# Performance work log

Hardware: AMD Instinct MI355X
Metric: run time of the kernel (lower is better)

Reference implementation:

```python
import jax, jax.numpy as jnp
import numpy as np

B, K, V, D, H, S, KS = 4, 4, 32, 64, 4, 1024, 5
GROUPS = K * V  # 128


def setup_inputs() -> dict:
    key = jax.random.key(0)
    k1, k2 = jax.random.split(key, 2)
    x = jax.random.normal(k1, (B, GROUPS * 3, S), dtype=jnp.float32)
    # grouped causal conv weight: (out_ch, in_ch_per_group, ks) = (K*V*D*3, 3, KS)
    W = jax.random.normal(k2, (GROUPS * D * 3, 3, KS), dtype=jnp.float32) * 0.05
    b = jnp.zeros((GROUPS * D * 3,), dtype=jnp.float32)
    return {"x": x, "W": W, "b": b}


def reference(x, W, b):
    temperature = 1.0
    dk = D // H
    # --- TCN (stand-in): causal grouped conv1d, groups = K*V ---
    xp = jnp.pad(x, ((0, 0), (0, 0), (KS - 1, 0)))  # left-pad for causality
    y = jax.lax.conv_general_dilated(
        xp, W, window_strides=(1,), padding='VALID',
        dimension_numbers=('NCH', 'OIH', 'NCH'),
        feature_group_count=GROUPS,
    ) + b[None, :, None]                      # (B, K*V*3*D, S)
    # channel layout per group is (3, D) to mirror torch reshape
    y = y.reshape(B * K, V, 3, D, S)
    q, k, v = y[:, :, 0], y[:, :, 1], y[:, :, 2]   # each (BK, V, D, S)
    q = q.reshape(B * K, V, H, dk, S)
    k = k.reshape(B * K, V, H, dk, S)
    v = v.reshape(B * K, V, H, dk, S)
    scale = (dk ** -0.5) / temperature
    # per-timestep attention over variables: (BK, H, S, Vq, Vk)
    logits = jnp.einsum('bqhds,bkhds->bhsqk', q, k) * scale
    attn = jax.nn.softmax(logits, axis=-1)
    # x_out[b,h,s,q,d] = sum_k attn * v  -> permute(0,3,1,4,2) layout (BK,V,H,dk,S)
    xo = jnp.einsum('bhsqk,bkhds->bqhds', attn, v)
    xo = xo.reshape(B * K, V * D, S).reshape(B, K * V * D, S)
    # mean over heads, to (BK, Vq, Vk, S) then (B, K, V, V, S)
    attn_m = jnp.transpose(attn.mean(axis=1), (0, 2, 3, 1)).reshape(B, K, V, V, S)
    return xo, attn_m
```

## Files before the change

### kernel.cpp

```cpp
#include <hip/hip_runtime.h>
#include <hip/hip_bf16.h>
#include <stdint.h>

#define SCALE 0.25f

typedef __attribute__((ext_vector_type(8))) short bf16x8;
typedef __attribute__((ext_vector_type(4))) float f32x4;
typedef __attribute__((ext_vector_type(16))) float f32x16;

__global__ __launch_bounds__(256) void prep_w2_kernel(const float* __restrict__ W,
                                                      float* __restrict__ W2) {
    int idx = blockIdx.x * 256 + threadIdx.x;
    int o = idx >> 4, j = idx & 15;
    W2[idx] = (j < 15) ? W[o * 15 + j] : 0.f;
}

#define XS_OFF 0
#define QK0_OFF 6912
#define QK1_OFF 23296
#define VT0_OFF 39680
#define VT1_OFF 49920
#define PT_OFF 60160
#define RING_OFF 80640
#define LDS_TOTAL 162880

__global__ __launch_bounds__(512) void fused4_kernel(const float* __restrict__ x,
                                                     const float* __restrict__ W2,
                                                     const float* __restrict__ bias,
                                                     float* __restrict__ out,
                                                     float* __restrict__ out_am) {
    extern __shared__ char smraw[];
    _Float16* xs = (_Float16*)(smraw + XS_OFF);
    unsigned short* pT = (unsigned short*)(smraw + PT_OFF);
    float* xo = (float*)(smraw + RING_OFF);
    float* att = (float*)smraw;

    int bi = blockIdx.x, slot = bi & 7, jj = bi >> 3;
    int k_ = slot >> 1, b = jj >> 4, st = ((slot & 1) << 4) | (jj & 15);
    int bk = b * 4 + k_;

    int t = threadIdx.x;
    int wid = t >> 6, lane = t & 63;
    int l31 = lane & 31, hi2 = lane >> 5;
    int l15 = lane & 15, hi4 = lane >> 4;

    int v = t >> 4, dk = t & 15;
    int g3 = (k_ * 32 + v) * 3;

    float w[3][16], bs[3];
    auto loadw = [&](int hh) {
        #pragma unroll
        for (int c3 = 0; c3 < 3; ++c3) {
            int row = (g3 + c3) * 64 + hh * 16 + dk;
            const float4* p = (const float4*)(W2 + (size_t)row * 16);
            float4 a0 = p[0], a1 = p[1], a2 = p[2], a3 = p[3];
            w[c3][0] = a0.x;  w[c3][1] = a0.y;  w[c3][2] = a0.z;  w[c3][3] = a0.w;
            w[c3][4] = a1.x;  w[c3][5] = a1.y;  w[c3][6] = a1.z;  w[c3][7] = a1.w;
            w[c3][8] = a2.x;  w[c3][9] = a2.y;  w[c3][10] = a2.z; w[c3][11] = a2.w;
            w[c3][12] = a3.x; w[c3][13] = a3.y; w[c3][14] = a3.z; w[c3][15] = a3.w;
            bs[c3] = bias[row];
        }
    };

    auto conv_stage = [&](int qs, int bufi) {
        __hip_bfloat16* qk = (__hip_bfloat16*)(smraw + (bufi ? QK1_OFF : QK0_OFF));
        __hip_bfloat16* vt = (__hip_bfloat16*)(smraw + (bufi ? VT1_OFF : VT0_OFF));
        float xw[3][12];
        #pragma unroll
        for (int i = 0; i < 3; ++i)
            #pragma unroll
            for (int j = 0; j < 12; ++j)
                xw[i][j] = (float)xs[(v * 3 + i) * 36 + qs * 8 + j];
        #pragma unroll
        for (int s8 = 0; s8 < 8; ++s8) {
            float a0 = bs[0], a1 = bs[1], a2 = bs[2];
            #pragma unroll
            for (int i = 0; i < 3; ++i)
                #pragma unroll
                for (int tt = 0; tt < 5; ++tt) {
                    float xv = xw[i][s8 + tt];
                    a0 = fmaf(xv, w[0][i * 5 + tt], a0);
                    a1 = fmaf(xv, w[1][i * 5 + tt], a1);
                    a2 = fmaf(xv, w[2][i * 5 + tt], a2);
                }
            qk[(s8 * 2 + 0) * 512 + v * 16 + dk] = __float2bfloat16(a0);
            qk[(s8 * 2 + 1) * 512 + v * 16 + dk] = __float2bfloat16(a1);
            vt[(s8 * 16 + dk) * 40 + v] = __float2bfloat16(a2);
        }
    };

    auto sweep = [&](int hp) {
        int rb = (32 * hp) % 40;
        int u = t >> 3;
        int s4 = (t & 7) * 4;
        #pragma unroll
        for (int j = 0; j < 8; ++j) {
            int c_loc = j * 64 + u;
            int col = c_loc ^ (4 * ((c_loc >> 4) & 7));
            float4 o;
            #pragma unroll
            for (int i2 = 0; i2 < 4; ++i2) {
                int r = rb + s4 + i2; if (r >= 40) r -= 40;
                (&o.x)[i2] = xo[r * 514 + col];
            }
            int qv = c_loc >> 4, dkc = c_loc & 15;
            int c = k_ * 2048 + qv * 64 + hp * 16 + dkc;
            *(float4*)(out + ((size_t)b * 8192 + c) * 1024 + st * 32 + s4) = o;
        }
    };

    float acc_am[4][16];
    #pragma unroll
    for (int a = 0; a < 4; ++a)
        #pragma unroll
        for (int r = 0; r < 16; ++r) acc_am[a][r] = 0.f;

    loadw(0);
    {
        int sbase = st * 32 - 4;
        #pragma unroll
        for (int i = 0; i < 7; ++i) {
            int idx = i * 512 + t;
            if (idx < 3456) {
                int row = idx / 36, col = idx - row * 36;
                int sg = sbase + col;
                float val = (sg >= 0) ? x[((size_t)b * 384 + k_ * 96 + row) * 1024 + sg] : 0.f;
                xs[idx] = (_Float16)val;
            }
        }
    }
    __syncthreads();
    conv_stage(0, 0);
    __syncthreads();

    for (int h = 0; h < 4; ++h) {
        #pragma unroll
        for (int q = 0; q < 4; ++q) {
            if (q == 3 && h < 3) loadw(h + 1);

            {
                const __hip_bfloat16* qk =
                    (const __hip_bfloat16*)(smraw + ((q & 1) ? QK1_OFF : QK0_OFF));
                const __hip_bfloat16* vt =
                    (const __hip_bfloat16*)(smraw + ((q & 1) ? VT1_OFF : VT0_OFF));
                const __hip_bfloat16* qb = qk + (wid * 2) * 512 + l31 * 16 + hi2 * 8;
                bf16x8 qf = *(const bf16x8*)qb;
                bf16x8 kf = *(const bf16x8*)(qb + 512);

                f32x16 zc;
                #pragma unroll
                for (int i = 0; i < 16; ++i) zc[i] = 0.f;
                f32x16 lg = __builtin_amdgcn_mfma_f32_32x32x16_bf16(kf, qf, zc, 0, 0, 0);

                float p[16], m = -3.0e38f;
                #pragma unroll
                for (int r = 0; r < 16; ++r) { p[r] = lg[r] * SCALE; m = fmaxf(m, p[r]); }
                m = fmaxf(m, __shfl_xor(m, 32));
                float ssum = 0.f;
                #pragma unroll
                for (int r = 0; r < 16; ++r) { p[r] = __expf(p[r] - m); ssum += p[r]; }
                ssum += __shfl_xor(ssum, 32);
                float inv = 1.f / ssum;
                #pragma unroll
                for (int r = 0; r < 16; ++r) { p[r] *= inv; acc_am[q][r] += p[r]; }

                unsigned* pTrow = (unsigned*)(pT + (size_t)(wid * 32 + l31) * 40);
                int wsw = (l31 >> 3) & 1 ? 4 : 0;
                #pragma unroll
                for (int mm = 0; mm < 8; ++mm) {
                    unsigned pk;
                    asm("v_cvt_pk_bf16_f32 %0, %1, %2"
                        : "=v"(pk) : "v"(p[2 * mm]), "v"(p[2 * mm + 1]));
                    pTrow[((mm & 1) + 4 * (mm >> 1) + 2 * hi2) ^ wsw] = pk;
                }

                int rsw = (l15 >> 3) & 1 ? 8 : 0;
                bf16x8 vf = *(const bf16x8*)&vt[(wid * 16 + l15) * 40 + hi4 * 8];
                bf16x8 p1 = *(const bf16x8*)&pT[(wid * 32 + l15) * 40 + (hi4 * 8 ^ rsw)];
                bf16x8 p2 = *(const bf16x8*)&pT[(wid * 32 + 16 + l15) * 40 + (hi4 * 8 ^ rsw)];
                f32x4 z4;
                #pragma unroll
                for (int i = 0; i < 4; ++i) z4[i] = 0.f;
                f32x4 xo1 = __builtin_amdgcn_mfma_f32_16x16x32_bf16(vf, p1, z4, 0, 0, 0);
                f32x4 xo2 = __builtin_amdgcn_mfma_f32_16x16x32_bf16(vf, p2, z4, 0, 0, 0);

                int rr = (32 * h + 8 * q + wid) % 40;
                float* row = xo + rr * 514;
                int sw = 4 * (l15 & 7);
                *(f32x4*)(row + ((l15 * 16 + hi4 * 4) ^ sw)) = xo1;
                *(f32x4*)(row + (((16 + l15) * 16 + hi4 * 4) ^ sw)) = xo2;
            }

            if (!(h == 3 && q == 3)) {
                conv_stage((q + 1) & 3, (q + 1) & 1);
            }

            if (q == 0 && h > 0) sweep(h - 1);

            __syncthreads();
        }
    }
    sweep(3);
    __syncthreads();

    #pragma unroll
    for (int pass = 0; pass < 2; ++pass) {
        if (pass) __syncthreads();
        if ((l31 >> 4) == pass) {
            int qh = l31 & 15;
            int csw = 4 * (qh & 7);
            #pragma unroll
            for (int q = 0; q < 4; ++q) {
                int sp = q * 8 + wid;
                int colp = sp ^ csw;
                #pragma unroll
                for (int r = 0; r < 16; ++r) {
                    int kv = (r & 3) + 8 * (r >> 2) + 4 * hi2;
                    att[(qh * 32 + kv) * 36 + colp] = 0.25f * acc_am[q][r];
                }
            }
        }
        __syncthreads();
        #pragma unroll
        for (int j = 0; j < 8; ++j) {
            int tr = j * 64 + (t >> 3);
            int csw = 4 * ((tr >> 5) & 7);
            int s4 = (t & 7) * 4;
            float4 o;
            o.x = att[tr * 36 + ((s4 + 0) ^ csw)];
            o.y = att[tr * 36 + ((s4 + 1) ^ csw)];
            o.z = att[tr * 36 + ((s4 + 2) ^ csw)];
            o.w = att[tr * 36 + ((s4 + 3) ^ csw)];
            *(float4*)(out_am + ((size_t)bk * 1024 + pass * 512 + tr) * 1024 + st * 32 + s4) = o;
        }
    }
}

extern "C" void kernel_launch(void* const* d_in, const int* in_sizes, int n_in,
                              void* d_out, int out_size, void* d_ws, size_t ws_size,
                              hipStream_t stream) {
    const float* x = (const float*)d_in[0];
    const float* W = (const float*)d_in[1];
    const float* bias = (const float*)d_in[2];
    float* out = (float*)d_out;
    float* out_am = out + (size_t)33554432;

    float* W2 = (float*)d_ws;

    (void)hipFuncSetAttribute((const void*)fused4_kernel,
                              hipFuncAttributeMaxDynamicSharedMemorySize, LDS_TOTAL);

    prep_w2_kernel<<<1536, 256, 0, stream>>>(W, W2);
    fused4_kernel<<<512, 512, LDS_TOTAL, stream>>>(x, W2, bias, out, out_am);
}
```

Baseline: 142.4 us.

## Move causal grouped conv onto bf16 MFMA with bias folded into weights

Replaces the scalar FMA convolution with 16x16x32 bf16 MFMA. Weights are pre-packed into bf16 with the bias folded in as an extra column multiplied by a constant 1.0, and x is staged as bf16. The loop is restructured into two halves of 16 timesteps per head with a single QK/VT buffer in place of double-buffered conv stages. The output ring buffer is stored as fp16 to shrink LDS use. This removes the VALU-heavy conv and weight register pressure, but lowers conv precision (bf16 inputs and weights) and the output staging precision, and adds extra barriers.

```diff
diff --git a/kernel.cpp b/kernel.cpp
--- a/kernel.cpp
+++ b/kernel.cpp
@@ -7,36 +7,49 @@
 typedef __attribute__((ext_vector_type(8))) short bf16x8;
 typedef __attribute__((ext_vector_type(4))) float f32x4;
 typedef __attribute__((ext_vector_type(16))) float f32x16;
-
-__global__ __launch_bounds__(256) void prep_w2_kernel(const float* __restrict__ W,
-                                                      float* __restrict__ W2) {
+typedef __fp16 fp16x4 __attribute__((ext_vector_type(4)));
+typedef unsigned int u32;
+typedef unsigned short u16;
+
+__global__ __launch_bounds__(256) void prep_wb_kernel(const float* __restrict__ W,
+                                                      const float* __restrict__ bias,
+                                                      __hip_bfloat16* __restrict__ Wb) {
     int idx = blockIdx.x * 256 + threadIdx.x;
-    int o = idx >> 4, j = idx & 15;
-    W2[idx] = (j < 15) ? W[o * 15 + j] : 0.f;
+    if (idx >= 786432) return;
+    int k = idx & 31; int r = idx >> 5;
+    int dkq = r & 15; r >>= 4;
+    int c3 = r % 3; r /= 3;
+    int h = r & 3; r >>= 2;
+    int v = r & 31; int kq = r >> 5;
+    int o = ((kq * 32 + v) * 3 + c3) * 64 + h * 16 + dkq;
+    float val = 0.f;
+    if (k < 15) val = W[o * 15 + k];
+    else if (k == 15) val = bias[o];
+    Wb[idx] = __float2bfloat16(val);
 }
 
-#define XS_OFF 0
-#define QK0_OFF 6912
-#define QK1_OFF 23296
-#define VT0_OFF 39680
-#define VT1_OFF 49920
-#define PT_OFF 60160
-#define RING_OFF 80640
-#define LDS_TOTAL 162880
-
-__global__ __launch_bounds__(512) void fused4_kernel(const float* __restrict__ x,
-                                                     const float* __restrict__ W2,
-                                                     const float* __restrict__ bias,
+#define QK_OFF   0
+#define VT_OFF   34304
+#define PT_OFF   54784
+#define XS_OFF   75264
+#define RING_OFF 82176
+#define LDS_TOTAL 132096
+#define QKSTRIDE 536
+
+__global__ __launch_bounds__(512) void fused8_kernel(const float* __restrict__ x,
+                                                     const __hip_bfloat16* __restrict__ Wb,
                                                      float* __restrict__ out,
                                                      float* __restrict__ out_am) {
     extern __shared__ char smraw[];
-    _Float16* xs = (_Float16*)(smraw + XS_OFF);
+    __hip_bfloat16* qk = (__hip_bfloat16*)(smraw + QK_OFF);
+    __hip_bfloat16* vt = (__hip_bfloat16*)(smraw + VT_OFF);
     unsigned short* pT = (unsigned short*)(smraw + PT_OFF);
-    float* xo = (float*)(smraw + RING_OFF);
+    u16* xs = (u16*)(smraw + XS_OFF);
+    __fp16* ring = (__fp16*)(smraw + RING_OFF);
     float* att = (float*)smraw;
 
-    int bi = blockIdx.x, slot = bi & 7, jj = bi >> 3;
-    int k_ = slot >> 1, b = jj >> 4, st = ((slot & 1) << 4) | (jj & 15);
+    int bi = blockIdx.x, slot = bi & 7, jj2 = bi >> 3;
+    int k_ = slot >> 1, b = jj2 >> 4, st = ((slot & 1) << 4) | (jj2 & 15);
     int bk = b * 4 + k_;
 
     int t = threadIdx.x;
@@ -44,78 +57,12 @@
     int l31 = lane & 31, hi2 = lane >> 5;
     int l15 = lane & 15, hi4 = lane >> 4;
 
-    int v = t >> 4, dk = t & 15;
-    int g3 = (k_ * 32 + v) * 3;
-
-    float w[3][16], bs[3];
-    auto loadw = [&](int hh) {
-        #pragma unroll
-        for (int c3 = 0; c3 < 3; ++c3) {
-            int row = (g3 + c3) * 64 + hh * 16 + dk;
-            const float4* p = (const float4*)(W2 + (size_t)row * 16);
-            float4 a0 = p[0], a1 = p[1], a2 = p[2], a3 = p[3];
-            w[c3][0] = a0.x;  w[c3][1] = a0.y;  w[c3][2] = a0.z;  w[c3][3] = a0.w;
-            w[c3][4] = a1.x;  w[c3][5] = a1.y;  w[c3][6] = a1.z;  w[c3][7] = a1.w;
-            w[c3][8] = a2.x;  w[c3][9] = a2.y;  w[c3][10] = a2.z; w[c3][11] = a2.w;
-            w[c3][12] = a3.x; w[c3][13] = a3.y; w[c3][14] = a3.z; w[c3][15] = a3.w;
-            bs[c3] = bias[row];
-        }
-    };
-
-    auto conv_stage = [&](int qs, int bufi) {
-        __hip_bfloat16* qk = (__hip_bfloat16*)(smraw + (bufi ? QK1_OFF : QK0_OFF));
-        __hip_bfloat16* vt = (__hip_bfloat16*)(smraw + (bufi ? VT1_OFF : VT0_OFF));
-        float xw[3][12];
-        #pragma unroll
-        for (int i = 0; i < 3; ++i)
-            #pragma unroll
-            for (int j = 0; j < 12; ++j)
-                xw[i][j] = (float)xs[(v * 3 + i) * 36 + qs * 8 + j];
-        #pragma unroll
-        for (int s8 = 0; s8 < 8; ++s8) {
-            float a0 = bs[0], a1 = bs[1], a2 = bs[2];
-            #pragma unroll
-            for (int i = 0; i < 3; ++i)
-                #pragma unroll
-                for (int tt = 0; tt < 5; ++tt) {
-                    float xv = xw[i][s8 + tt];
-                    a0 = fmaf(xv, w[0][i * 5 + tt], a0);
-                    a1 = fmaf(xv, w[1][i * 5 + tt], a1);
-                    a2 = fmaf(xv, w[2][i * 5 + tt], a2);
-                }
-            qk[(s8 * 2 + 0) * 512 + v * 16 + dk] = __float2bfloat16(a0);
-            qk[(s8 * 2 + 1) * 512 + v * 16 + dk] = __float2bfloat16(a1);
-            vt[(s8 * 16 + dk) * 40 + v] = __float2bfloat16(a2);
-        }
-    };
-
-    auto sweep = [&](int hp) {
-        int rb = (32 * hp) % 40;
-        int u = t >> 3;
-        int s4 = (t & 7) * 4;
-        #pragma unroll
-        for (int j = 0; j < 8; ++j) {
-            int c_loc = j * 64 + u;
-            int col = c_loc ^ (4 * ((c_loc >> 4) & 7));
-            float4 o;
-            #pragma unroll
-            for (int i2 = 0; i2 < 4; ++i2) {
-                int r = rb + s4 + i2; if (r >= 40) r -= 40;
-                (&o.x)[i2] = xo[r * 514 + col];
-            }
-            int qv = c_loc >> 4, dkc = c_loc & 15;
-            int c = k_ * 2048 + qv * 64 + hp * 16 + dkc;
-            *(float4*)(out + ((size_t)b * 8192 + c) * 1024 + st * 32 + s4) = o;
-        }
-    };
-
     float acc_am[4][16];
     #pragma unroll
     for (int a = 0; a < 4; ++a)
         #pragma unroll
         for (int r = 0; r < 16; ++r) acc_am[a][r] = 0.f;
 
-    loadw(0);
     {
         int sbase = st * 32 - 4;
         #pragma unroll
@@ -125,27 +72,82 @@
                 int row = idx / 36, col = idx - row * 36;
                 int sg = sbase + col;
                 float val = (sg >= 0) ? x[((size_t)b * 384 + k_ * 96 + row) * 1024 + sg] : 0.f;
-                xs[idx] = (_Float16)val;
+                __hip_bfloat16 bv = __float2bfloat16(val);
+                xs[idx] = *(u16*)&bv;
             }
         }
     }
     __syncthreads();
-    conv_stage(0, 0);
-    __syncthreads();
+
+    auto sweep = [&](int hp) {
+        int rb = (32 * hp) % 48;
+        int u = t >> 3, s4 = (t & 7) * 4;
+        #pragma unroll
+        for (int j = 0; j < 8; ++j) {
+            int c_loc = j * 64 + u;
+            float4 o;
+            #pragma unroll
+            for (int i2 = 0; i2 < 4; ++i2) {
+                int rr = rb + s4 + i2; if (rr >= 48) rr -= 48;
+                (&o.x)[i2] = (float)ring[rr * 520 + c_loc];
+            }
+            int c = k_ * 2048 + (c_loc >> 4) * 64 + hp * 16 + (c_loc & 15);
+            *(float4*)(out + ((size_t)b * 8192 + c) * 1024 + st * 32 + s4) = o;
+        }
+    };
+
+    f32x4 z4;
+    #pragma unroll
+    for (int i = 0; i < 4; ++i) z4[i] = 0.f;
 
     for (int h = 0; h < 4; ++h) {
         #pragma unroll
-        for (int q = 0; q < 4; ++q) {
-            if (q == 3 && h < 3) loadw(h + 1);
-
-            {
-                const __hip_bfloat16* qk =
-                    (const __hip_bfloat16*)(smraw + ((q & 1) ? QK1_OFF : QK0_OFF));
-                const __hip_bfloat16* vt =
-                    (const __hip_bfloat16*)(smraw + ((q & 1) ? VT1_OFF : VT0_OFF));
-                const __hip_bfloat16* qb = qk + (wid * 2) * 512 + l31 * 16 + hi2 * 8;
+        for (int half = 0; half < 2; ++half) {
+            #pragma unroll
+            for (int vv = 0; vv < 4; ++vv) {
+                int v = wid * 4 + vv;
+                const __hip_bfloat16* wbase =
+                    Wb + (size_t)((((k_ * 32 + v) * 4 + h) * 3) * 16) * 32;
+                bf16x8 wr0 = *(const bf16x8*)(wbase + (0 * 16 + l15) * 32 + hi4 * 8);
+                bf16x8 wr1 = *(const bf16x8*)(wbase + (1 * 16 + l15) * 32 + hi4 * 8);
+                bf16x8 wr2 = *(const bf16x8*)(wbase + (2 * 16 + l15) * 32 + hi4 * 8);
+                bf16x8 xf;
+                #pragma unroll
+                for (int j = 0; j < 8; ++j) xf[j] = 0;
+                {
+                    int cix = half * 16 + l15;
+                    const u16* x0 = xs + (3 * v) * 36 + cix;
+                    const u16* x1 = x0 + 36;
+                    const u16* x2 = x0 + 72;
+                    if (hi4 == 0) {
+                        xf[0] = x0[0]; xf[1] = x0[1]; xf[2] = x0[2]; xf[3] = x0[3]; xf[4] = x0[4];
+                        xf[5] = x1[0]; xf[6] = x1[1]; xf[7] = x1[2];
+                    } else if (hi4 == 1) {
+                        xf[0] = x1[3]; xf[1] = x1[4];
+                        xf[2] = x2[0]; xf[3] = x2[1]; xf[4] = x2[2]; xf[5] = x2[3]; xf[6] = x2[4];
+                        xf[7] = (short)0x3F80;
+                    }
+                }
+                f32x4 d0 = __builtin_amdgcn_mfma_f32_16x16x32_bf16(wr0, xf, z4, 0, 0, 0);
+                f32x4 d1 = __builtin_amdgcn_mfma_f32_16x16x32_bf16(wr1, xf, z4, 0, 0, 0);
+                f32x4 d2 = __builtin_amdgcn_mfma_f32_16x16x32_bf16(wr2, xf, z4, 0, 0, 0);
+
+                #pragma unroll
+                for (int i2 = 0; i2 < 4; ++i2) {
+                    int dk = 4 * hi4 + i2;
+                    qk[(l15 * 2 + 0) * QKSTRIDE + v * 16 + dk] = __float2bfloat16(d0[i2]);
+                    qk[(l15 * 2 + 1) * QKSTRIDE + v * 16 + dk] = __float2bfloat16(d1[i2]);
+                    vt[(l15 * 16 + dk) * 40 + v] = __float2bfloat16(d2[i2]);
+                }
+            }
+            __syncthreads();
+
+            #pragma unroll
+            for (int jj = 0; jj < 2; ++jj) {
+                int s_tile = wid * 2 + jj;
+                const __hip_bfloat16* qb = qk + (s_tile * 2) * QKSTRIDE + l31 * 16 + hi2 * 8;
                 bf16x8 qf = *(const bf16x8*)qb;
-                bf16x8 kf = *(const bf16x8*)(qb + 512);
+                bf16x8 kf = *(const bf16x8*)(qb + QKSTRIDE);
 
                 f32x16 zc;
                 #pragma unroll
@@ -161,8 +163,9 @@
                 for (int r = 0; r < 16; ++r) { p[r] = __expf(p[r] - m); ssum += p[r]; }
                 ssum += __shfl_xor(ssum, 32);
                 float inv = 1.f / ssum;
-                #pragma unroll
-                for (int r = 0; r < 16; ++r) { p[r] *= inv; acc_am[q][r] += p[r]; }
+                int a_idx = half * 2 + jj;
+                #pragma unroll
+                for (int r = 0; r < 16; ++r) { p[r] *= inv; acc_am[a_idx][r] += p[r]; }
 
                 unsigned* pTrow = (unsigned*)(pT + (size_t)(wid * 32 + l31) * 40);
                 int wsw = (l31 >> 3) & 1 ? 4 : 0;
@@ -175,33 +178,30 @@
                 }
 
                 int rsw = (l15 >> 3) & 1 ? 8 : 0;
-                bf16x8 vf = *(const bf16x8*)&vt[(wid * 16 + l15) * 40 + hi4 * 8];
+                bf16x8 vf = *(const bf16x8*)(vt + (s_tile * 16 + l15) * 40 + hi4 * 8);
                 bf16x8 p1 = *(const bf16x8*)&pT[(wid * 32 + l15) * 40 + (hi4 * 8 ^ rsw)];
                 bf16x8 p2 = *(const bf16x8*)&pT[(wid * 32 + 16 + l15) * 40 + (hi4 * 8 ^ rsw)];
-                f32x4 z4;
-                #pragma unroll
-                for (int i = 0; i < 4; ++i) z4[i] = 0.f;
                 f32x4 xo1 = __builtin_amdgcn_mfma_f32_16x16x32_bf16(vf, p1, z4, 0, 0, 0);
                 f32x4 xo2 = __builtin_amdgcn_mfma_f32_16x16x32_bf16(vf, p2, z4, 0, 0, 0);
 
-                int rr = (32 * h + 8 * q + wid) % 40;
-                float* row = xo + rr * 514;
-                int sw = 4 * (l15 & 7);
-                *(f32x4*)(row + ((l15 * 16 + hi4 * 4) ^ sw)) = xo1;
-                *(f32x4*)(row + (((16 + l15) * 16 + hi4 * 4) ^ sw)) = xo2;
-            }
-
-            if (!(h == 3 && q == 3)) {
-                conv_stage((q + 1) & 3, (q + 1) & 1);
-            }
-
-            if (q == 0 && h > 0) sweep(h - 1);
+                int rr = (32 * h + half * 16 + s_tile) % 48;
+                __fp16* rowp = ring + rr * 520;
+                fp16x4 e1, e2;
+                #pragma unroll
+                for (int i2 = 0; i2 < 4; ++i2) {
+                    e1[i2] = (__fp16)xo1[i2];
+                    e2[i2] = (__fp16)xo2[i2];
+                }
+                *(fp16x4*)(rowp + l15 * 16 + hi4 * 4) = e1;
+                *(fp16x4*)(rowp + (16 + l15) * 16 + hi4 * 4) = e2;
+            }
+
+            if (half == 0 && h > 0) sweep(h - 1);
 
             __syncthreads();
         }
     }
     sweep(3);
-    __syncthreads();
 
     #pragma unroll
     for (int pass = 0; pass < 2; ++pass) {
@@ -210,13 +210,13 @@
             int qh = l31 & 15;
             int csw = 4 * (qh & 7);
             #pragma unroll
-            for (int q = 0; q < 4; ++q) {
-                int sp = q * 8 + wid;
+            for (int a = 0; a < 4; ++a) {
+                int sp = (a >> 1) * 16 + wid * 2 + (a & 1);
                 int colp = sp ^ csw;
                 #pragma unroll
                 for (int r = 0; r < 16; ++r) {
                     int kv = (r & 3) + 8 * (r >> 2) + 4 * hi2;
-                    att[(qh * 32 + kv) * 36 + colp] = 0.25f * acc_am[q][r];
+                    att[(qh * 32 + kv) * 36 + colp] = 0.25f * acc_am[a][r];
                 }
             }
         }
@@ -245,11 +245,11 @@
     float* out = (float*)d_out;
     float* out_am = out + (size_t)33554432;
 
-    float* W2 = (float*)d_ws;
-
-    (void)hipFuncSetAttribute((const void*)fused4_kernel,
+    __hip_bfloat16* Wb = (__hip_bfloat16*)d_ws;
+
+    (void)hipFuncSetAttribute((const void*)fused8_kernel,
                               hipFuncAttributeMaxDynamicSharedMemorySize, LDS_TOTAL);
 
-    prep_w2_kernel<<<1536, 256, 0, stream>>>(W, W2);
-    fused4_kernel<<<512, 512, LDS_TOTAL, stream>>>(x, W2, bias, out, out_am);
+    prep_wb_kernel<<<3072, 256, 0, stream>>>(W, bias, Wb);
+    fused8_kernel<<<512, 512, LDS_TOTAL, stream>>>(x, Wb, out, out_am);
 }
```

After: 123.2 us. -13.5%, faster.
